# Performance work log

Measured on AMD Instinct MI355X. Metric: run time of the kernel, lower is better.

The kernel has to match this reference:

```python
import math
import jax, jax.numpy as jnp
import numpy as np

LEVELS = 4          # wavelet_levels
PRUNE = 0.05        # wavelet_packet_prune_ratio
EPS = 1e-6
SQRT2 = math.sqrt(2.0)


def _haar_split(c):
    n = c.shape[-1]
    if n % 2 != 0:
        c = jnp.concatenate([c, jnp.zeros(c.shape[:-1] + (1,), c.dtype)], axis=-1)
    even, odd = c[..., 0::2], c[..., 1::2]
    return (even + odd) / SQRT2, (even - odd) / SQRT2, n


def _haar_merge(low, high, orig):
    even = (low + high) / SQRT2
    odd = (low - high) / SQRT2
    out = jnp.stack([even, odd], axis=-1).reshape(*low.shape[:-1], low.shape[-1] * 2)
    return out[..., :orig]


def _coherence(c, gpu):
    unit = c / jnp.maximum(jnp.abs(c), EPS)
    return jnp.clip(jnp.abs(jnp.mean(unit * jnp.conj(gpu), axis=-1, keepdims=True)), 0.0, 1.0)


def _cost(c, gpu):
    # gauge-aware packet cost: Shannon entropy of energy distribution + (1 - coherence)
    if c.shape[-1] <= 1:
        return jnp.float32(0.0)
    e = jnp.square(jnp.abs(c))
    p = jnp.maximum(e / jnp.maximum(e.sum(-1, keepdims=True), EPS), EPS)
    ent = -(p * jnp.log(p)).sum(-1)
    coh = _coherence(c, gpu)[..., 0]
    return jax.lax.stop_gradient(jnp.mean(ent + (1.0 - coh)))


def _band_center(path):
    if not path:
        return 0.0
    idx = 0
    for b in path:
        idx = (idx << 1) | b
    return (idx + 0.5) / (2 ** len(path))


def _leaf_gain(c, path, depth, gpu, Wp, bp, Wo, bo, lfg, sigma, hfg, cutoff):
    mag = jnp.maximum(jnp.abs(c), EPS)
    phase = jnp.arctan2(c.imag, c.real) / math.pi
    nle = jnp.broadcast_to(
        jnp.log(jnp.maximum(jnp.mean(jnp.square(jnp.abs(c)), -1, keepdims=True), EPS)), mag.shape)
    dn = jnp.full(mag.shape, depth / max(1, LEVELS), mag.dtype)
    bcv = _band_center(path)
    bc = jnp.full(mag.shape, bcv, mag.dtype)
    coh = jnp.broadcast_to(_coherence(c, gpu), mag.shape)
    pos = jnp.broadcast_to(jnp.linspace(0.0, 1.0, c.shape[-1], dtype=mag.dtype), mag.shape)
    feats = jnp.stack([jnp.log(mag), phase, nle, dn, bc, coh, pos], axis=-1)  # [..., n, 7]
    gd = jax.nn.silu(feats @ Wp.T + bp) @ Wo.T + bo                            # [..., n, 2]
    dm = 0.25 * jnp.tanh(gd[..., 0])
    dp = 0.5 * math.pi * jnp.tanh(gd[..., 1])
    lbb = 1.0 + lfg * jnp.exp(-(bcv * bcv) / jnp.square(sigma))
    hbd = hfg + (1.0 - hfg) * jax.nn.sigmoid((cutoff - bcv) / sigma)
    gm = lbb * hbd * (1.0 + lfg * coh) * (hfg + (1.0 - hfg) * coh) * jnp.exp(dm)
    return jax.lax.complex(gm * jnp.cos(dp), gm * jnp.sin(dp))  # torch.polar


def _filter_leaf(c, path, depth, total_e, gpu, params):
    Wp, bp, Wo, bo, lfg, sigma, hfg, cutoff = params
    node_e = jax.lax.stop_gradient(jnp.square(jnp.abs(c)).sum())
    filtered = c * _leaf_gain(c, path, depth, gpu, Wp, bp, Wo, bo, lfg, sigma, hfg, cutoff)
    coh_v = jax.lax.stop_gradient(jnp.mean(_coherence(c, gpu)))
    # spectral subtraction
    fm = jnp.abs(filtered)
    nf = jnp.median(fm, axis=-1, keepdims=True)
    damping = hfg + (1.0 - hfg) * jax.nn.sigmoid((cutoff - _band_center(path)) / sigma)
    den = jax.nn.relu(fm - (1.0 - damping) * nf)
    filtered = den * (filtered / jnp.maximum(fm, EPS))
    # prune low-energy / low-coherence leaves
    prune = jnp.logical_or(node_e / total_e < PRUNE, coh_v < PRUNE)
    return jnp.where(prune, filtered * jnp.square(hfg), filtered)


def _apply_node(c, depth, path, total_e, gpu, params):
    cost = _cost(c, gpu)
    leaf = _filter_leaf(c, path, depth, total_e, gpu, params)
    if depth >= LEVELS or c.shape[-1] <= 1:
        return leaf, cost
    low, high, orig = _haar_split(c)
    lr, lc = _apply_node(low, depth + 1, path + (0,), total_e, gpu, params)
    hr, hc = _apply_node(high, depth + 1, path + (1,), total_e, gpu, params)
    merged = _haar_merge(lr, hr, orig)
    child_cost = lc + hc
    # best-basis selection (wavelet_packet_best_basis=True)
    out = jnp.where(child_cost < cost, merged, leaf)
    return out, jnp.minimum(child_cost, cost)


def setup_inputs() -> dict:
    key = jax.random.key(0)
    ks = jax.random.split(key, 3)
    B, R, N = 8, 64, 8192
    x = jax.random.normal(ks[0], (B, R, N), jnp.float32)
    Wp = jax.random.normal(ks[1], (12, 7), jnp.float32) * math.sqrt(2.0 / 19.0)  # xavier-ish
    bp = jnp.zeros((12,), jnp.float32)
    Wo = jax.random.normal(ks[2], (2, 12), jnp.float32) * 0.1
    bo = jnp.zeros((2,), jnp.float32)
    return {"x": x, "Wp": Wp, "bp": bp, "Wo": Wo, "bo": bo,
            "lfg": jnp.float32(0.5), "sigma": jnp.float32(0.3),
            "hfg": jnp.float32(0.7), "cutoff": jnp.float32(0.25)}


def reference(x, Wp, bp, Wo, bo, lfg, sigma, hfg, cutoff):
    n = x.shape[-1]
    spec = jnp.fft.fft(x)  # complex64 [B, R, N]
    # _fft_filter spectral gating
    r2 = jnp.square(jnp.fft.fftfreq(n).astype(x.dtype))
    lfb = 1.0 + lfg * jnp.exp(-r2 / jnp.square(sigma))
    radius = jnp.sqrt(r2 + 1e-12)
    gate = jax.nn.sigmoid((cutoff - radius) / jnp.maximum(sigma, 0.05))
    spec = spec * (lfb * (hfg + (1.0 - hfg) * gate))
    # global phase unit
    unit = spec / jnp.maximum(jnp.abs(spec), EPS)
    g = jnp.mean(unit, axis=-1, keepdims=True)
    gpu = g / jnp.maximum(jnp.abs(g), EPS)
    total_e = jax.lax.stop_gradient(jnp.square(jnp.abs(spec)).sum())
    params = (Wp, bp, Wo, bo, lfg, sigma, hfg, cutoff)
    out, _ = _apply_node(spec, 0, (), total_e, gpu, params)
    return jnp.fft.ifft(out).real
```

## Files before the change

kernel.cpp:

```cpp
#include <hip/hip_runtime.h>
#include <hip/hip_fp16.h>
#include <math.h>

#define NN      8192
#define LOGN    13
#define ROWS    512
#define NT      512
#define NNODES  31
#define EPSF    1e-6f
#define PRUNEF  0.05f
#define SQRT1_2F 0.70710678118654752f
#define PIF      3.14159265358979323f
#define INV_PIF  0.31830988618379067f
#define HALF_PIF 1.57079632679489662f

typedef unsigned int uint;

__device__ __forceinline__ float fast_rcp(float x){ return __builtin_amdgcn_rcpf(x); }
__device__ __forceinline__ float fast_rsq(float x){ return __builtin_amdgcn_rsqf(x); }

__device__ __forceinline__ float tanh_fast(float x){
    float e = __expf(2.f * x);
    return 1.f - 2.f * fast_rcp(e + 1.f);
}
__device__ __forceinline__ float silu_pade(float h){
    float y = fminf(3.f, fmaxf(-3.f, 0.5f * h));
    float y2 = y * y;
    float num = y * fmaf(y2, 10.f, 105.f);
    float den = fmaf(y2, 45.f, fmaf(y2 * y2, 1.f, 105.f));
    return 0.5f * h * (1.f + num * fast_rcp(den));
}
__device__ __forceinline__ float exp_small(float z){
    return fmaf(z, fmaf(z, fmaf(z, fmaf(z, 0.041666667f, 0.16666667f), 0.5f), 1.f), 1.f);
}

__device__ __forceinline__ float fast_atan2f(float y, float x) {
    float ay = fabsf(y), ax = fabsf(x);
    float mx = fmaxf(ax, ay), mn = fminf(ax, ay);
    float a = (mx > 0.f) ? (mn * fast_rcp(mx)) : 0.f;
    bool big = a > 0.4142135679f;
    float t = big ? ((a - 1.f) * fast_rcp(a + 1.f)) : a;
    float z2 = t * t;
    float p = fmaf(8.05374449538e-2f, z2, -1.38776856032e-1f);
    p = fmaf(p, z2, 1.99777106478e-1f);
    p = fmaf(p, z2, -3.33329491539e-1f);
    float r = fmaf(p * z2, t, t);
    if (big) r += 0.78539816339744831f;
    if (ay > ax) r = 1.57079632679489662f - r;
    if (x < 0.f) r = 3.14159265358979323f - r;
    return copysignf(r, y);
}

__device__ __forceinline__ float2 cmul(float2 a, float2 b){
    return make_float2(a.x*b.x - a.y*b.y, a.x*b.y + a.y*b.x);
}
__device__ __forceinline__ float2 cadd(float2 a, float2 b){ return make_float2(a.x+b.x, a.y+b.y); }
__device__ __forceinline__ float2 csub(float2 a, float2 b){ return make_float2(a.x-b.x, a.y-b.y); }

__device__ __forceinline__ uint pack_h2(float2 v){
    __half2 h = __floats2half2_rn(v.x, v.y);
    return __builtin_bit_cast(uint, h);
}
__device__ __forceinline__ float2 unpack_h2(uint u){
    __half2 h = __builtin_bit_cast(__half2, u);
    return make_float2(__low2float(h), __high2float(h));
}

__device__ __forceinline__ void wave_red8(float* a) {
    #pragma unroll
    for (int m = 32; m >= 1; m >>= 1) {
        #pragma unroll
        for (int q = 0; q < 8; ++q) a[q] += __shfl_xor(a[q], m);
    }
}

__global__ __launch_bounds__(NT, 4) void k_pre(
    const float* __restrict__ x, uint* __restrict__ Lv16,
    float* __restrict__ Se, float* __restrict__ Coh, float* __restrict__ Ent,
    const float* lfg_p, const float* sig_p, const float* hfg_p, const float* cut_p)
{
    __shared__ float2 sh[NN];
    __shared__ float4 wred[8];
    __shared__ float nacc[16][4];
    int row = blockIdx.x, tid = threadIdx.x;
    float lfg = *lfg_p, sigma = *sig_p, hfg = *hfg_p, cutoff = *cut_p;

    const float* xr = x + ((size_t)row << LOGN);
    #pragma unroll
    for (int t = 0; t < 16; ++t) {
        int i = tid + (t << 9);
        sh[i] = make_float2(xr[i], 0.f);
    }
    __syncthreads();

    for (int sp = 0; sp < 6; ++sp) {
        int lg = 11 - 2 * sp;
        int Hh = 1 << lg;
        float angf = -PIF / (float)(2 * Hh);
        #pragma unroll 4
        for (int c = 0; c < 4; ++c) {
            int q = tid + (c << 9);
            int j = q & (Hh - 1);
            int p = ((q >> lg) << (lg + 2)) | j;
            float2 a = sh[p], b = sh[p + Hh], cc = sh[p + 2 * Hh], d = sh[p + 3 * Hh];
            float ang = angf * (float)j;
            float s = __sinf(ang), co = __cosf(ang);
            float2 t1 = make_float2(co, s);
            float2 t2 = make_float2(co * co - s * s, 2.f * co * s);
            float2 a1 = cadd(a, cc);
            float2 c1 = cmul(csub(a, cc), t1);
            float2 b1 = cadd(b, d);
            float2 u  = cmul(csub(b, d), t1);
            float2 d1 = make_float2(u.y, -u.x);
            sh[p]          = cadd(a1, b1);
            sh[p + Hh]     = cmul(csub(a1, b1), t2);
            sh[p + 2 * Hh] = cadd(c1, d1);
            sh[p + 3 * Hh] = cmul(csub(c1, d1), t2);
        }
        __syncthreads();
    }
    #pragma unroll 8
    for (int c = 0; c < 8; ++c) {
        int p = (tid + (c << 9)) << 1;
        float2 a = sh[p], b = sh[p + 1];
        sh[p] = cadd(a, b);
        sh[p + 1] = csub(a, b);
    }
    __syncthreads();

    float inv_gs = 1.f / fmaxf(sigma, 0.05f);
    float is2 = 1.f / (sigma * sigma);
    float se = 0.f, slg = 0.f, sux = 0.f, suy = 0.f;
    #pragma unroll
    for (int t = 0; t < 16; ++t) {
        int p = tid + (t << 9);
        int k = (int)(__brev((uint)p) >> 19);
        float fk = (k < NN / 2) ? (float)k : (float)(k - NN);
        float f = fk * (1.0f / (float)NN);
        float r2 = f * f;
        float lfb = 1.f + lfg * __expf(-r2 * is2);
        float radius = sqrtf(r2 + 1e-12f);
        float gate = fast_rcp(1.f + __expf(-(cutoff - radius) * inv_gs));
        float mult = lfb * (hfg + (1.f - hfg) * gate);
        float2 c = sh[p];
        c.x *= mult; c.y *= mult;
        sh[p] = c;
        float e = fmaf(c.x, c.x, c.y * c.y);
        se += e;
        slg += e * __logf(fmaxf(e, 1e-30f));
        float inv = fminf(fast_rsq(e), 1e6f);
        sux += c.x * inv; suy += c.y * inv;
    }
    #pragma unroll
    for (int m = 32; m >= 1; m >>= 1) {
        se += __shfl_xor(se, m); slg += __shfl_xor(slg, m);
        sux += __shfl_xor(sux, m); suy += __shfl_xor(suy, m);
    }
    if ((tid & 63) == 0) wred[tid >> 6] = make_float4(se, slg, sux, suy);
    __syncthreads();
    if (tid == 0) {
        float4 r = wred[0];
        #pragma unroll
        for (int w = 1; w < 8; ++w) {
            r.x += wred[w].x; r.y += wred[w].y; r.z += wred[w].z; r.w += wred[w].w;
        }
        float gx = r.z / (float)NN, gy = r.w / (float)NN;
        float ga = sqrtf(gx * gx + gy * gy);
        float denom = fmaxf(r.x, EPSF);
        Se[row]  = r.x;
        Ent[row] = __logf(denom) - r.y / denom;
        Coh[row] = fminf(ga, 1.f);
    }

    for (int dp = 0; dp < 4; ++dp) {
        int shn = 12 - dp;
        int h = 1 << shn;
        int fim1 = (1 << (3 - dp)) - 1;
        if (tid < 64) ((float*)nacc)[tid] = 0.f;
        __syncthreads();
        float acc[8] = {0,0,0,0,0,0,0,0};
        #pragma unroll
        for (int t = 0; t < 8; ++t) {
            int q = tid + (t << 9);
            int p = ((q & ~(h - 1)) << 1) | (q & (h - 1));
            float2 a = sh[p], b = sh[p + h];
            float2 lo = make_float2((a.x + b.x) * SQRT1_2F, (a.y + b.y) * SQRT1_2F);
            float2 hi = make_float2((a.x - b.x) * SQRT1_2F, (a.y - b.y) * SQRT1_2F);
            sh[p] = lo; sh[p + h] = hi;
            float e1 = fmaf(lo.x, lo.x, lo.y * lo.y);
            acc[0] += e1; acc[1] += e1 * __logf(fmaxf(e1, 1e-30f));
            float i1 = fminf(fast_rsq(e1), 1e6f);
            acc[2] += lo.x * i1; acc[3] += lo.y * i1;
            float e2 = fmaf(hi.x, hi.x, hi.y * hi.y);
            acc[4] += e2; acc[5] += e2 * __logf(fmaxf(e2, 1e-30f));
            float i2 = fminf(fast_rsq(e2), 1e6f);
            acc[6] += hi.x * i2; acc[7] += hi.y * i2;
            if (((t + 1) & fim1) == 0) {
                wave_red8(acc);
                if ((tid & 63) == 0) {
                    int ca = (q >> shn) << 1;
                    atomicAdd(&nacc[ca][0], acc[0]);   atomicAdd(&nacc[ca][1], acc[1]);
                    atomicAdd(&nacc[ca][2], acc[2]);   atomicAdd(&nacc[ca][3], acc[3]);
                    atomicAdd(&nacc[ca+1][0], acc[4]); atomicAdd(&nacc[ca+1][1], acc[5]);
                    atomicAdd(&nacc[ca+1][2], acc[6]); atomicAdd(&nacc[ca+1][3], acc[7]);
                }
                #pragma unroll
                for (int qq = 0; qq < 8; ++qq) acc[qq] = 0.f;
            }
        }
        __syncthreads();
        int cn = 2 << dp;
        if (tid < cn) {
            float E = nacc[tid][0], SL = nacc[tid][1], ZX = nacc[tid][2], ZY = nacc[tid][3];
            float denom = fmaxf(E, EPSF);
            float ent = __logf(denom) - SL / denom;
            float invn = 1.f / (float)(1 << shn);
            float zx = ZX * invn, zy = ZY * invn;
            float ch = fminf(sqrtf(zx * zx + zy * zy), 1.f);
            int g = cn - 1 + tid;
            Se[g * ROWS + row] = E; Coh[g * ROWS + row] = ch; Ent[g * ROWS + row] = ent;
        }
        __syncthreads();
    }

    uint* lrow = Lv16 + ((size_t)row << LOGN);
    #pragma unroll
    for (int t = 0; t < 16; ++t) {
        int k = tid + (t << 9);
        lrow[k] = pack_h2(sh[k]);
    }
}

__global__ __launch_bounds__(NT) void k_decide(
    const float* __restrict__ Se, const float* __restrict__ Coh, const float* __restrict__ Ent,
    int* __restrict__ fFg, int* __restrict__ fPg)
{
    __shared__ float dtmp[3 * NNODES];
    __shared__ int fF[NNODES], fP[NNODES];
    int tid = threadIdx.x;
    float* dcost = dtmp; float* dne = dtmp + NNODES; float* dcm = dtmp + 2 * NNODES;
    int wid = tid >> 6, lane = tid & 63;
    for (int gn = wid; gn < NNODES; gn += 8) {
        float a = 0.f, b = 0.f, cc = 0.f;
        #pragma unroll
        for (int rr = 0; rr < ROWS / 64; ++rr) {
            int r = lane + (rr << 6);
            float ch = Coh[gn * ROWS + r];
            a += Ent[gn * ROWS + r] + 1.f - ch;
            b += Se[gn * ROWS + r];
            cc += ch;
        }
        #pragma unroll
        for (int m = 32; m >= 1; m >>= 1) {
            a += __shfl_xor(a, m); b += __shfl_xor(b, m); cc += __shfl_xor(cc, m);
        }
        if (lane == 0) { dcost[gn] = a / (float)ROWS; dne[gn] = b; dcm[gn] = cc / (float)ROWS; }
    }
    __syncthreads();
    if (tid == 0) {
        float mc[NNODES]; int sel[NNODES]; int act[NNODES];
        for (int gn = NNODES - 1; gn >= 0; --gn) {
            if (gn >= 15) { mc[gn] = dcost[gn]; sel[gn] = 0; }
            else {
                float chc = mc[2 * gn + 1] + mc[2 * gn + 2];
                sel[gn] = (chc < dcost[gn]) ? 1 : 0;
                mc[gn] = fminf(chc, dcost[gn]);
            }
        }
        float total_e = dne[0];
        act[0] = 1;
        for (int gn = 1; gn < NNODES; ++gn) {
            int p = (gn - 1) >> 1;
            act[gn] = act[p] && sel[p];
        }
        for (int gn = 0; gn < NNODES; ++gn) {
            int isleaf = (gn >= 15);
            fF[gn] = (act[gn] && (isleaf || !sel[gn])) ? 1 : 0;
            fP[gn] = ((dne[gn] / total_e < PRUNEF) || (dcm[gn] < PRUNEF)) ? 1 : 0;
        }
    }
    __syncthreads();
    if (tid < NNODES) { fFg[tid] = fF[tid]; fPg[tid] = fP[tid]; }
}

__device__ __forceinline__ uint key_at(const float2* sh, int p) {
    float2 v = sh[p];
    return __float_as_uint(fmaf(v.x, v.x, v.y * v.y));
}

__device__ __forceinline__ uint2 hist_locate1024(
    const uint* hist, int tid, uint r, uint* wsum, uint* selres)
{
    uint l0 = hist[2 * tid], l1 = hist[2 * tid + 1];
    uint s = l0 + l1;
    uint sc = s;
    #pragma unroll
    for (int o = 1; o < 64; o <<= 1) {
        uint v = __shfl_up(sc, o);
        if ((tid & 63) >= o) sc += v;
    }
    int wid = tid >> 6;
    if ((tid & 63) == 63) wsum[wid] = sc;
    __syncthreads();
    uint wb = 0;
    #pragma unroll
    for (int w = 0; w < 8; ++w) if (w < wid) wb += wsum[w];
    uint c0 = wb + sc - s;
    if (r >= c0 && r < c0 + l0) { selres[0] = 2u * tid;      selres[1] = c0; }
    c0 += l0;
    if (r >= c0 && r < c0 + l1) { selres[0] = 2u * tid + 1u; selres[1] = c0; }
    __syncthreads();
    uint2 res = make_uint2(selres[0], selres[1]);
    __syncthreads();
    return res;
}

template<int EPT>
__device__ __forceinline__ float median_node(
    const float2* sh, int nd, int tid,
    uint* hist, uint* wsum, uint* selres)
{
    uint r1 = (uint)(nd / 2 - 1), r2 = (uint)(nd / 2);
    for (int k = tid; k < 1024; k += NT) hist[k] = 0u;
    __syncthreads();
    #pragma unroll
    for (int c = 0; c < EPT; ++c)
        atomicAdd(&hist[key_at(sh, tid + (c << 9)) >> 21], 1u);
    __syncthreads();
    uint2 A1 = hist_locate1024(hist, tid, r1, wsum, selres);
    uint2 A2 = hist_locate1024(hist, tid, r2, wsum, selres);
    uint va, vb;
    if (A1.x != A2.x) {
        if (tid == 0) { selres[0] = 0u; selres[1] = 0xFFFFFFFFu; }
        __syncthreads();
        #pragma unroll
        for (int c = 0; c < EPT; ++c) {
            uint k = key_at(sh, tid + (c << 9));
            uint b = k >> 21;
            if (b == A1.x) atomicMax(&selres[0], k);
            if (b == A2.x) atomicMin(&selres[1], k);
        }
        __syncthreads();
        va = selres[0]; vb = selres[1];
        __syncthreads();
    } else {
        uint p1 = A1.x;
        for (int k = tid; k < 1024; k += NT) hist[k] = 0u;
        __syncthreads();
        #pragma unroll
        for (int c = 0; c < EPT; ++c) {
            uint k = key_at(sh, tid + (c << 9));
            if ((k >> 21) == p1) atomicAdd(&hist[(k >> 11) & 1023u], 1u);
        }
        __syncthreads();
        uint2 B1 = hist_locate1024(hist, tid, r1 - A1.y, wsum, selres);
        uint2 B2 = hist_locate1024(hist, tid, r2 - A1.y, wsum, selres);
        if (B1.x != B2.x) {
            uint pA = (p1 << 10) | B1.x, pB = (p1 << 10) | B2.x;
            if (tid == 0) { selres[0] = 0u; selres[1] = 0xFFFFFFFFu; }
            __syncthreads();
            #pragma unroll
            for (int c = 0; c < EPT; ++c) {
                uint k = key_at(sh, tid + (c << 9));
                uint b = k >> 11;
                if (b == pA) atomicMax(&selres[0], k);
                if (b == pB) atomicMin(&selres[1], k);
            }
            __syncthreads();
            va = selres[0]; vb = selres[1];
            __syncthreads();
        } else {
            uint pfx = (p1 << 10) | B1.x;
            for (int k = tid; k < 1024; k += NT) hist[k] = 0u;
            __syncthreads();
            #pragma unroll
            for (int c = 0; c < EPT; ++c) {
                uint k = key_at(sh, tid + (c << 9));
                if ((k >> 11) == pfx) atomicAdd(&hist[(k >> 1) & 1023u], 1u);
            }
            __syncthreads();
            uint2 C1 = hist_locate1024(hist, tid, r1 - A1.y - B1.y, wsum, selres);
            uint2 C2 = hist_locate1024(hist, tid, r2 - A1.y - B1.y, wsum, selres);
            va = ((pfx << 10) | C1.x) << 1;
            vb = ((pfx << 10) | C2.x) << 1;
        }
    }
    return 0.5f * (sqrtf(__uint_as_float(va)) + sqrtf(__uint_as_float(vb)));
}

template<int D>
__device__ __forceinline__ void filter_node_reg(
    float2 (&v)[16], int n, int tid, float2* sh,
    const float* __restrict__ Wp, const float* __restrict__ bp,
    const float* __restrict__ Wo, const float* __restrict__ bo,
    const float* __restrict__ Se, const float* __restrict__ Coh,
    const int* __restrict__ fPg, int row,
    uint* hist, uint* wsum, uint* selres,
    float lfg, float sigma, float hfg, float cutoff)
{
    constexpr int CNT = 16 >> D;
    constexpr int ND  = NN >> D;
    constexpr int EPT = ND >> 9;
    int g = (1 << D) - 1 + n;

    #pragma unroll
    for (int t = 0; t < 16; ++t) {
        int k = t - n * CNT;
        if ((unsigned)k < (unsigned)CNT) sh[tid + (k << 9)] = v[t];
    }
    __syncthreads();

    float bcv = (D == 0) ? 0.f : ((float)n + 0.5f) / (float)(1 << D);
    float coh = Coh[g * ROWS + row];
    float sev = Se[g * ROWS + row];
    float nle = __logf(fmaxf(sev * (1.f / (float)ND), EPSF));
    float dnv = (float)D * 0.25f;
    float lbb = 1.f + lfg * __expf(-(bcv * bcv) / (sigma * sigma));
    float hbd = hfg + (1.f - hfg) * fast_rcp(1.f + __expf(-(cutoff - bcv) / sigma));
    float gbase = lbb * hbd * (1.f + lfg * coh) * (hfg + (1.f - hfg) * coh);
    float invnm1 = 1.f / (float)(ND - 1);
    float hb[12];
    #pragma unroll
    for (int j = 0; j < 12; ++j)
        hb[j] = bp[j] + nle * Wp[j*7+2] + dnv * Wp[j*7+3] + bcv * Wp[j*7+4] + coh * Wp[j*7+5];
    float bo0 = bo[0], bo1 = bo[1];

    #pragma unroll
    for (int c = 0; c < EPT; ++c) {
        int o = tid + (c << 9);
        float2 cv = sh[o];
        float m2 = fmaf(cv.x, cv.x, cv.y * cv.y);
        float f0 = 0.5f * __logf(fmaxf(m2, 1e-12f));
        float f1 = fast_atan2f(cv.y, cv.x) * INV_PIF;
        int itrue = (int)(__brev((uint)o) >> (19 + D));
        float f6 = (float)itrue * invnm1;
        float acc0 = bo0, acc1 = bo1;
        #pragma unroll
        for (int j = 0; j < 12; ++j) {
            float h = fmaf(f0, Wp[j*7], fmaf(f1, Wp[j*7+1], fmaf(f6, Wp[j*7+6], hb[j])));
            float s = silu_pade(h);
            acc0 = fmaf(s, Wo[j], acc0);
            acc1 = fmaf(s, Wo[12 + j], acc1);
        }
        float gm = gbase * exp_small(0.25f * tanh_fast(acc0));
        float dph = HALF_PIF * tanh_fast(acc1);
        float spv, cpv;
        __sincosf(dph, &spv, &cpv);
        float fr = gm * (cv.x * cpv - cv.y * spv);
        float fi = gm * (cv.x * spv + cv.y * cpv);
        sh[o] = make_float2(fr, fi);
    }
    __syncthreads();

    float nf = median_node<EPT>(sh, ND, tid, hist, wsum, selres);
    float thr = (1.f - hbd) * nf;
    float pf = fPg[g] ? (hfg * hfg) : 1.f;

    #pragma unroll
    for (int c = 0; c < EPT; ++c) {
        int o = tid + (c << 9);
        float2 w = sh[o];
        float fm = sqrtf(fmaf(w.x, w.x, w.y * w.y));
        float den = fmaxf(fm - thr, 0.f);
        float s = den * fast_rcp(fmaxf(fm, EPSF)) * pf;
        sh[o] = make_float2(w.x * s, w.y * s);
    }
    __syncthreads();

    #pragma unroll
    for (int t = 0; t < 16; ++t) {
        int k = t - n * CNT;
        if ((unsigned)k < (unsigned)CNT) v[t] = sh[tid + (k << 9)];
    }
    __syncthreads();
}

template<int DT>
__device__ __forceinline__ void merge_reg(float2 (&v)[16]){
    #pragma unroll
    for (int t = 0; t < 16; ++t) {
        if ((t & DT) == 0) {
            float2 lo = v[t], hi = v[t + DT];
            v[t]      = make_float2((lo.x + hi.x) * SQRT1_2F, (lo.y + hi.y) * SQRT1_2F);
            v[t + DT] = make_float2((lo.x - hi.x) * SQRT1_2F, (lo.y - hi.y) * SQRT1_2F);
        }
    }
}

__global__ __launch_bounds__(NT, 4) void k_rest(
    const uint* __restrict__ Lv16,
    const float* __restrict__ Se, const float* __restrict__ Coh,
    const int* __restrict__ fFg, const int* __restrict__ fPg,
    float* __restrict__ out,
    const float* __restrict__ Wp, const float* __restrict__ bp,
    const float* __restrict__ Wo, const float* __restrict__ bo,
    const float* lfg_p, const float* sig_p, const float* hfg_p, const float* cut_p)
{
    __shared__ float2 sh[NN];
    __shared__ __align__(16) uint hist[1024];
    __shared__ uint wsum[8];
    __shared__ uint selres[2];

    int row = blockIdx.x, tid = threadIdx.x;
    float lfg = *lfg_p, sigma = *sig_p, hfg = *hfg_p, cutoff = *cut_p;

    const uint* lr = Lv16 + ((size_t)row << LOGN);
    uint raw[16];
    #pragma unroll
    for (int t = 0; t < 16; ++t) raw[t] = lr[tid + (t << 9)];

    float2 v[16];
    #pragma unroll
    for (int t = 0; t < 16; ++t) v[t] = unpack_h2(raw[t]);

    for (int n = 0; n < 16; ++n)
        if (fFg[15 + n])
            filter_node_reg<4>(v, n, tid, sh, Wp, bp, Wo, bo, Se, Coh, fPg, row, hist, wsum, selres, lfg, sigma, hfg, cutoff);

    merge_reg<1>(v);
    for (int n = 0; n < 8; ++n)
        if (fFg[7 + n])
            filter_node_reg<3>(v, n, tid, sh, Wp, bp, Wo, bo, Se, Coh, fPg, row, hist, wsum, selres, lfg, sigma, hfg, cutoff);
    merge_reg<2>(v);
    for (int n = 0; n < 4; ++n)
        if (fFg[3 + n])
            filter_node_reg<2>(v, n, tid, sh, Wp, bp, Wo, bo, Se, Coh, fPg, row, hist, wsum, selres, lfg, sigma, hfg, cutoff);
    merge_reg<4>(v);
    for (int n = 0; n < 2; ++n)
        if (fFg[1 + n])
            filter_node_reg<1>(v, n, tid, sh, Wp, bp, Wo, bo, Se, Coh, fPg, row, hist, wsum, selres, lfg, sigma, hfg, cutoff);
    merge_reg<8>(v);
    if (fFg[0])
        filter_node_reg<0>(v, 0, tid, sh, Wp, bp, Wo, bo, Se, Coh, fPg, row, hist, wsum, selres, lfg, sigma, hfg, cutoff);

    #pragma unroll
    for (int t = 0; t < 16; ++t) sh[tid + (t << 9)] = v[t];
    __syncthreads();

    for (int sp = 0; sp < 6; ++sp) {
        int h = 1 << (2 * sp);
        float angf = PIF / (float)(2 * h);
        #pragma unroll 4
        for (int c = 0; c < 4; ++c) {
            int q = tid + (c << 9);
            int jj = q & (h - 1);
            int p0 = ((q >> (2 * sp)) << (2 * sp + 2)) | jj;
            float ang = angf * (float)jj;
            float s2 = __sinf(ang), c2 = __cosf(ang);
            float2 t2 = make_float2(c2, s2);
            float2 t1 = make_float2(c2 * c2 - s2 * s2, 2.f * c2 * s2);
            float2 a = sh[p0], b = sh[p0 + h], cc = sh[p0 + 2 * h], d = sh[p0 + 3 * h];
            float2 tb = cmul(t1, b);
            float2 ap = cadd(a, tb), bp2 = csub(a, tb);
            float2 td = cmul(t1, d);
            float2 cp = cadd(cc, td), dp2 = csub(cc, td);
            float2 tc = cmul(t2, cp);
            float2 u  = cmul(t2, dp2);
            float2 iB = make_float2(-u.y, u.x);
            sh[p0]         = cadd(ap, tc);
            sh[p0 + h]     = cadd(bp2, iB);
            sh[p0 + 2 * h] = csub(ap, tc);
            sh[p0 + 3 * h] = csub(bp2, iB);
        }
        __syncthreads();
    }
    {
        float angf = PIF / 4096.f;
        #pragma unroll 8
        for (int c = 0; c < 8; ++c) {
            int p = tid + (c << 9);
            float ang = angf * (float)p;
            float s = __sinf(ang), co = __cosf(ang);
            float2 a = sh[p], b = sh[p + 4096];
            float2 tb = cmul(make_float2(co, s), b);
            sh[p] = cadd(a, tb);
            sh[p + 4096] = csub(a, tb);
        }
        __syncthreads();
    }
    float* orow = out + ((size_t)row << LOGN);
    #pragma unroll
    for (int t = 0; t < 16; ++t) {
        int i = tid + (t << 9);
        orow[i] = sh[i].x * (1.0f / (float)NN);
    }
}

extern "C" void kernel_launch(void* const* d_in, const int* in_sizes, int n_in,
                              void* d_out, int out_size, void* d_ws, size_t ws_size,
                              hipStream_t stream) {
    const float* x   = (const float*)d_in[0];
    const float* Wp  = (const float*)d_in[1];
    const float* bp  = (const float*)d_in[2];
    const float* Wo  = (const float*)d_in[3];
    const float* bo  = (const float*)d_in[4];
    const float* lfg = (const float*)d_in[5];
    const float* sig = (const float*)d_in[6];
    const float* hfg = (const float*)d_in[7];
    const float* cut = (const float*)d_in[8];
    float* out = (float*)d_out;

    size_t LVB = (size_t)ROWS * NN * sizeof(uint);
    char* ws = (char*)d_ws;
    uint*   Lv16 = (uint*)ws;
    float*  Se   = (float*)(ws + LVB);
    float*  Coh  = Se  + (size_t)NNODES * ROWS;
    float*  Ent  = Coh + (size_t)NNODES * ROWS;
    int*    fFg  = (int*)(Ent + (size_t)NNODES * ROWS);
    int*    fPg  = fFg + NNODES;
    size_t need = (size_t)((char*)(fPg + NNODES) - ws);
    if (ws_size < need) return;

    dim3 b(NT);
    k_pre   <<<dim3(ROWS), b, 0, stream>>>(x, Lv16, Se, Coh, Ent, lfg, sig, hfg, cut);
    k_decide<<<dim3(1),    b, 0, stream>>>(Se, Coh, Ent, fFg, fPg);
    k_rest  <<<dim3(ROWS), b, 0, stream>>>(Lv16, Se, Coh, fFg, fPg, out, Wp, bp, Wo, bo, lfg, sig, hfg, cut);
}
```

Baseline: 139.8 us.

## Keep wavelet split stats in registers and filter root node without shared memory

The k_pre packet-split statistics now run on per-thread register arrays, with one barrier at the end instead of several shared-memory passes per level. The root-node filter in k_rest works on registers directly, using a register-based median histogram instead of staging through shared memory. tanh and sincos are replaced with Pade and polynomial approximations. This removes shared-memory traffic and barriers, at the cost of more register pressure and small accuracy changes from the approximations.

```diff
diff --git a/kernel.cpp b/kernel.cpp
--- a/kernel.cpp
+++ b/kernel.cpp
@@ -19,9 +19,12 @@
 __device__ __forceinline__ float fast_rcp(float x){ return __builtin_amdgcn_rcpf(x); }
 __device__ __forceinline__ float fast_rsq(float x){ return __builtin_amdgcn_rsqf(x); }
 
-__device__ __forceinline__ float tanh_fast(float x){
-    float e = __expf(2.f * x);
-    return 1.f - 2.f * fast_rcp(e + 1.f);
+__device__ __forceinline__ float tanh_pade(float y){
+    y = fminf(3.f, fmaxf(-3.f, y));
+    float y2 = y * y;
+    float num = y * fmaf(y2, 10.f, 105.f);
+    float den = fmaf(y2, 45.f, fmaf(y2 * y2, 1.f, 105.f));
+    return num * fast_rcp(den);
 }
 __device__ __forceinline__ float silu_pade(float h){
     float y = fminf(3.f, fmaxf(-3.f, 0.5f * h));
@@ -32,6 +35,14 @@
 }
 __device__ __forceinline__ float exp_small(float z){
     return fmaf(z, fmaf(z, fmaf(z, fmaf(z, 0.041666667f, 0.16666667f), 0.5f), 1.f), 1.f);
+}
+__device__ __forceinline__ float sin_halfpi(float t){
+    float t2 = t * t;
+    return t * fmaf(t2, fmaf(t2, fmaf(t2, -4.6817541e-3f, 7.96926262e-2f), -6.45964097e-1f), 1.57079632f);
+}
+__device__ __forceinline__ float cos_halfpi(float t){
+    float t2 = t * t;
+    return fmaf(t2, fmaf(t2, fmaf(t2, fmaf(t2, 9.1937e-4f, -2.08634807e-2f), 2.53669508e-1f), -1.23370055f), 1.f);
 }
 
 __device__ __forceinline__ float fast_atan2f(float y, float x) {
@@ -74,6 +85,52 @@
     }
 }
 
+template<int DP>
+__device__ __forceinline__ void level_split_stats(
+    float2 (&v)[16], float* nacc, int tid)
+{
+    constexpr int ST = 8 >> DP;
+    #pragma unroll
+    for (int t = 0; t < 16; ++t) {
+        if ((t & ST) == 0) {
+            float2 a = v[t], b = v[t + ST];
+            v[t]      = make_float2((a.x + b.x) * SQRT1_2F, (a.y + b.y) * SQRT1_2F);
+            v[t + ST] = make_float2((a.x - b.x) * SQRT1_2F, (a.y - b.y) * SQRT1_2F);
+        }
+    }
+    constexpr int CNT = 16 >> (DP + 1);
+    constexpr int NPAIR = 1 << DP;
+    constexpr int G0 = (2 << DP) - 1;
+    #pragma unroll
+    for (int pr = 0; pr < NPAIR; ++pr) {
+        float acc[8] = {0,0,0,0,0,0,0,0};
+        #pragma unroll
+        for (int s = 0; s < CNT; ++s) {
+            float2 w = v[(2 * pr) * CNT + s];
+            float e = fmaf(w.x, w.x, w.y * w.y);
+            acc[0] += e; acc[1] += e * __logf(fmaxf(e, 1e-30f));
+            float iv = fminf(fast_rsq(e), 1e6f);
+            acc[2] += w.x * iv; acc[3] += w.y * iv;
+        }
+        #pragma unroll
+        for (int s = 0; s < CNT; ++s) {
+            float2 w = v[(2 * pr + 1) * CNT + s];
+            float e = fmaf(w.x, w.x, w.y * w.y);
+            acc[4] += e; acc[5] += e * __logf(fmaxf(e, 1e-30f));
+            float iv = fminf(fast_rsq(e), 1e6f);
+            acc[6] += w.x * iv; acc[7] += w.y * iv;
+        }
+        wave_red8(acc);
+        if ((tid & 63) == 0) {
+            int ga = G0 + 2 * pr, gb = ga + 1;
+            atomicAdd(&nacc[(ga - 1) * 4 + 0], acc[0]); atomicAdd(&nacc[(ga - 1) * 4 + 1], acc[1]);
+            atomicAdd(&nacc[(ga - 1) * 4 + 2], acc[2]); atomicAdd(&nacc[(ga - 1) * 4 + 3], acc[3]);
+            atomicAdd(&nacc[(gb - 1) * 4 + 0], acc[4]); atomicAdd(&nacc[(gb - 1) * 4 + 1], acc[5]);
+            atomicAdd(&nacc[(gb - 1) * 4 + 2], acc[6]); atomicAdd(&nacc[(gb - 1) * 4 + 3], acc[7]);
+        }
+    }
+}
+
 __global__ __launch_bounds__(NT, 4) void k_pre(
     const float* __restrict__ x, uint* __restrict__ Lv16,
     float* __restrict__ Se, float* __restrict__ Coh, float* __restrict__ Ent,
@@ -81,7 +138,7 @@
 {
     __shared__ float2 sh[NN];
     __shared__ float4 wred[8];
-    __shared__ float nacc[16][4];
+    __shared__ float nacc[30 * 4];
     int row = blockIdx.x, tid = threadIdx.x;
     float lfg = *lfg_p, sigma = *sig_p, hfg = *hfg_p, cutoff = *cut_p;
 
@@ -128,9 +185,11 @@
     }
     __syncthreads();
 
+    if (tid < 120) nacc[tid] = 0.f;
     float inv_gs = 1.f / fmaxf(sigma, 0.05f);
     float is2 = 1.f / (sigma * sigma);
     float se = 0.f, slg = 0.f, sux = 0.f, suy = 0.f;
+    float2 v[16];
     #pragma unroll
     for (int t = 0; t < 16; ++t) {
         int p = tid + (t << 9);
@@ -144,7 +203,7 @@
         float mult = lfb * (hfg + (1.f - hfg) * gate);
         float2 c = sh[p];
         c.x *= mult; c.y *= mult;
-        sh[p] = c;
+        v[t] = c;
         float e = fmaf(c.x, c.x, c.y * c.y);
         se += e;
         slg += e * __logf(fmaxf(e, 1e-30f));
@@ -172,63 +231,28 @@
         Coh[row] = fminf(ga, 1.f);
     }
 
-    for (int dp = 0; dp < 4; ++dp) {
-        int shn = 12 - dp;
-        int h = 1 << shn;
-        int fim1 = (1 << (3 - dp)) - 1;
-        if (tid < 64) ((float*)nacc)[tid] = 0.f;
-        __syncthreads();
-        float acc[8] = {0,0,0,0,0,0,0,0};
-        #pragma unroll
-        for (int t = 0; t < 8; ++t) {
-            int q = tid + (t << 9);
-            int p = ((q & ~(h - 1)) << 1) | (q & (h - 1));
-            float2 a = sh[p], b = sh[p + h];
-            float2 lo = make_float2((a.x + b.x) * SQRT1_2F, (a.y + b.y) * SQRT1_2F);
-            float2 hi = make_float2((a.x - b.x) * SQRT1_2F, (a.y - b.y) * SQRT1_2F);
-            sh[p] = lo; sh[p + h] = hi;
-            float e1 = fmaf(lo.x, lo.x, lo.y * lo.y);
-            acc[0] += e1; acc[1] += e1 * __logf(fmaxf(e1, 1e-30f));
-            float i1 = fminf(fast_rsq(e1), 1e6f);
-            acc[2] += lo.x * i1; acc[3] += lo.y * i1;
-            float e2 = fmaf(hi.x, hi.x, hi.y * hi.y);
-            acc[4] += e2; acc[5] += e2 * __logf(fmaxf(e2, 1e-30f));
-            float i2 = fminf(fast_rsq(e2), 1e6f);
-            acc[6] += hi.x * i2; acc[7] += hi.y * i2;
-            if (((t + 1) & fim1) == 0) {
-                wave_red8(acc);
-                if ((tid & 63) == 0) {
-                    int ca = (q >> shn) << 1;
-                    atomicAdd(&nacc[ca][0], acc[0]);   atomicAdd(&nacc[ca][1], acc[1]);
-                    atomicAdd(&nacc[ca][2], acc[2]);   atomicAdd(&nacc[ca][3], acc[3]);
-                    atomicAdd(&nacc[ca+1][0], acc[4]); atomicAdd(&nacc[ca+1][1], acc[5]);
-                    atomicAdd(&nacc[ca+1][2], acc[6]); atomicAdd(&nacc[ca+1][3], acc[7]);
-                }
-                #pragma unroll
-                for (int qq = 0; qq < 8; ++qq) acc[qq] = 0.f;
-            }
-        }
-        __syncthreads();
-        int cn = 2 << dp;
-        if (tid < cn) {
-            float E = nacc[tid][0], SL = nacc[tid][1], ZX = nacc[tid][2], ZY = nacc[tid][3];
-            float denom = fmaxf(E, EPSF);
-            float ent = __logf(denom) - SL / denom;
-            float invn = 1.f / (float)(1 << shn);
-            float zx = ZX * invn, zy = ZY * invn;
-            float ch = fminf(sqrtf(zx * zx + zy * zy), 1.f);
-            int g = cn - 1 + tid;
-            Se[g * ROWS + row] = E; Coh[g * ROWS + row] = ch; Ent[g * ROWS + row] = ent;
-        }
-        __syncthreads();
+    level_split_stats<0>(v, nacc, tid);
+    level_split_stats<1>(v, nacc, tid);
+    level_split_stats<2>(v, nacc, tid);
+    level_split_stats<3>(v, nacc, tid);
+    __syncthreads();
+    if (tid < 30) {
+        int g = tid + 1;
+        float E = nacc[tid * 4 + 0], SL = nacc[tid * 4 + 1];
+        float ZX = nacc[tid * 4 + 2], ZY = nacc[tid * 4 + 3];
+        float denom = fmaxf(E, EPSF);
+        float ent = __logf(denom) - SL / denom;
+        int d = 31 - __clz(g + 1);
+        float invn = 1.f / (float)(NN >> d);
+        float zx = ZX * invn, zy = ZY * invn;
+        float ch = fminf(sqrtf(zx * zx + zy * zy), 1.f);
+        Se[g * ROWS + row] = E; Coh[g * ROWS + row] = ch; Ent[g * ROWS + row] = ent;
     }
 
     uint* lrow = Lv16 + ((size_t)row << LOGN);
     #pragma unroll
-    for (int t = 0; t < 16; ++t) {
-        int k = tid + (t << 9);
-        lrow[k] = pack_h2(sh[k]);
-    }
+    for (int t = 0; t < 16; ++t)
+        lrow[tid + (t << 9)] = pack_h2(v[t]);
 }
 
 __global__ __launch_bounds__(NT) void k_decide(
@@ -283,10 +307,10 @@
     if (tid < NNODES) { fFg[tid] = fF[tid]; fPg[tid] = fP[tid]; }
 }
 
-__device__ __forceinline__ uint key_at(const float2* sh, int p) {
-    float2 v = sh[p];
+__device__ __forceinline__ uint key_of(float2 v) {
     return __float_as_uint(fmaf(v.x, v.x, v.y * v.y));
 }
+__device__ __forceinline__ uint key_at(const float2* sh, int p) { return key_of(sh[p]); }
 
 __device__ __forceinline__ uint2 hist_locate1024(
     const uint* hist, int tid, uint r, uint* wsum, uint* selres)
@@ -388,8 +412,130 @@
     return 0.5f * (sqrtf(__uint_as_float(va)) + sqrtf(__uint_as_float(vb)));
 }
 
+__device__ __forceinline__ float median_root_reg(
+    const float2 (&v)[16], int tid, uint* hist, uint* wsum, uint* selres)
+{
+    const uint r1 = NN / 2 - 1, r2 = NN / 2;
+    for (int k = tid; k < 1024; k += NT) hist[k] = 0u;
+    __syncthreads();
+    #pragma unroll
+    for (int t = 0; t < 16; ++t)
+        atomicAdd(&hist[key_of(v[t]) >> 21], 1u);
+    __syncthreads();
+    uint2 A1 = hist_locate1024(hist, tid, r1, wsum, selres);
+    uint2 A2 = hist_locate1024(hist, tid, r2, wsum, selres);
+    uint va, vb;
+    if (A1.x != A2.x) {
+        if (tid == 0) { selres[0] = 0u; selres[1] = 0xFFFFFFFFu; }
+        __syncthreads();
+        #pragma unroll
+        for (int t = 0; t < 16; ++t) {
+            uint k = key_of(v[t]);
+            uint b = k >> 21;
+            if (b == A1.x) atomicMax(&selres[0], k);
+            if (b == A2.x) atomicMin(&selres[1], k);
+        }
+        __syncthreads();
+        va = selres[0]; vb = selres[1];
+        __syncthreads();
+    } else {
+        uint p1 = A1.x;
+        for (int k = tid; k < 1024; k += NT) hist[k] = 0u;
+        __syncthreads();
+        #pragma unroll
+        for (int t = 0; t < 16; ++t) {
+            uint k = key_of(v[t]);
+            if ((k >> 21) == p1) atomicAdd(&hist[(k >> 11) & 1023u], 1u);
+        }
+        __syncthreads();
+        uint2 B1 = hist_locate1024(hist, tid, r1 - A1.y, wsum, selres);
+        uint2 B2 = hist_locate1024(hist, tid, r2 - A1.y, wsum, selres);
+        if (B1.x != B2.x) {
+            uint pA = (p1 << 10) | B1.x, pB = (p1 << 10) | B2.x;
+            if (tid == 0) { selres[0] = 0u; selres[1] = 0xFFFFFFFFu; }
+            __syncthreads();
+            #pragma unroll
+            for (int t = 0; t < 16; ++t) {
+                uint k = key_of(v[t]);
+                uint b = k >> 11;
+                if (b == pA) atomicMax(&selres[0], k);
+                if (b == pB) atomicMin(&selres[1], k);
+            }
+            __syncthreads();
+            va = selres[0]; vb = selres[1];
+            __syncthreads();
+        } else {
+            uint pfx = (p1 << 10) | B1.x;
+            for (int k = tid; k < 1024; k += NT) hist[k] = 0u;
+            __syncthreads();
+            #pragma unroll
+            for (int t = 0; t < 16; ++t) {
+                uint k = key_of(v[t]);
+                if ((k >> 11) == pfx) atomicAdd(&hist[(k >> 1) & 1023u], 1u);
+            }
+            __syncthreads();
+            uint2 C1 = hist_locate1024(hist, tid, r1 - A1.y - B1.y, wsum, selres);
+            uint2 C2 = hist_locate1024(hist, tid, r2 - A1.y - B1.y, wsum, selres);
+            va = ((pfx << 10) | C1.x) << 1;
+            vb = ((pfx << 10) | C2.x) << 1;
+        }
+    }
+    return 0.5f * (sqrtf(__uint_as_float(va)) + sqrtf(__uint_as_float(vb)));
+}
+
+struct NodeConst {
+    float hbd, gbase, hb[12], bo0, bo1;
+};
+__device__ __forceinline__ NodeConst node_consts(
+    int D, int nodes, int n, int g, int ND, int row,
+    const float* __restrict__ Wp, const float* __restrict__ bp,
+    const float* __restrict__ Wo, const float* __restrict__ bo,
+    const float* __restrict__ Se, const float* __restrict__ Coh,
+    float lfg, float sigma, float hfg, float cutoff, float& coh_o)
+{
+    NodeConst nc;
+    float bcv = (D == 0) ? 0.f : ((float)n + 0.5f) / (float)nodes;
+    float coh = Coh[g * ROWS + row];
+    float sev = Se[g * ROWS + row];
+    float nle = __logf(fmaxf(sev * (1.f / (float)ND), EPSF));
+    float dnv = (float)D * 0.25f;
+    float lbb = 1.f + lfg * __expf(-(bcv * bcv) / (sigma * sigma));
+    nc.hbd = hfg + (1.f - hfg) * fast_rcp(1.f + __expf(-(cutoff - bcv) / sigma));
+    nc.gbase = lbb * nc.hbd * (1.f + lfg * coh) * (hfg + (1.f - hfg) * coh);
+    #pragma unroll
+    for (int j = 0; j < 12; ++j)
+        nc.hb[j] = bp[j] + nle * Wp[j*7+2] + dnv * Wp[j*7+3] + bcv * Wp[j*7+4] + coh * Wp[j*7+5];
+    nc.bo0 = bo[0]; nc.bo1 = bo[1];
+    coh_o = coh;
+    return nc;
+}
+
+__device__ __forceinline__ float2 mlp_apply(
+    float2 cv, int o, int D, float invnm1, const NodeConst& nc,
+    const float* __restrict__ Wp, const float* __restrict__ Wo)
+{
+    float m2 = fmaf(cv.x, cv.x, cv.y * cv.y);
+    float f0 = 0.5f * __logf(fmaxf(m2, 1e-12f));
+    float f1 = fast_atan2f(cv.y, cv.x) * INV_PIF;
+    int itrue = (int)(__brev((uint)o) >> (19 + D));
+    float f6 = (float)itrue * invnm1;
+    float acc0 = nc.bo0, acc1 = nc.bo1;
+    #pragma unroll
+    for (int j = 0; j < 12; ++j) {
+        float h = fmaf(f0, Wp[j*7], fmaf(f1, Wp[j*7+1], fmaf(f6, Wp[j*7+6], nc.hb[j])));
+        float s = silu_pade(h);
+        acc0 = fmaf(s, Wo[j], acc0);
+        acc1 = fmaf(s, Wo[12 + j], acc1);
+    }
+    float gm = nc.gbase * exp_small(0.25f * tanh_pade(acc0));
+    float tp = tanh_pade(acc1);
+    float spv = sin_halfpi(tp), cpv = cos_halfpi(tp);
+    return make_float2(gm * (cv.x * cpv - cv.y * spv),
+                       gm * (cv.x * spv + cv.y * cpv));
+}
+
 template<int D>
-__device__ __forceinline__ void filter_node_reg(
+__device__ __forceinline__ void filter_node_sh(
     float2 (&v)[16], int n, int tid, float2* sh,
     const float* __restrict__ Wp, const float* __restrict__ bp,
     const float* __restrict__ Wo, const float* __restrict__ bo,
@@ -410,50 +556,20 @@
     }
     __syncthreads();
 
-    float bcv = (D == 0) ? 0.f : ((float)n + 0.5f) / (float)(1 << D);
-    float coh = Coh[g * ROWS + row];
-    float sev = Se[g * ROWS + row];
-    float nle = __logf(fmaxf(sev * (1.f / (float)ND), EPSF));
-    float dnv = (float)D * 0.25f;
-    float lbb = 1.f + lfg * __expf(-(bcv * bcv) / (sigma * sigma));
-    float hbd = hfg + (1.f - hfg) * fast_rcp(1.f + __expf(-(cutoff - bcv) / sigma));
-    float gbase = lbb * hbd * (1.f + lfg * coh) * (hfg + (1.f - hfg) * coh);
+    float coh;
+    NodeConst nc = node_consts(D, 1 << D, n, g, ND, row, Wp, bp, Wo, bo, Se, Coh,
+                               lfg, sigma, hfg, cutoff, coh);
     float invnm1 = 1.f / (float)(ND - 1);
-    float hb[12];
-    #pragma unroll
-    for (int j = 0; j < 12; ++j)
-        hb[j] = bp[j] + nle * Wp[j*7+2] + dnv * Wp[j*7+3] + bcv * Wp[j*7+4] + coh * Wp[j*7+5];
-    float bo0 = bo[0], bo1 = bo[1];
 
     #pragma unroll
     for (int c = 0; c < EPT; ++c) {
         int o = tid + (c << 9);
-        float2 cv = sh[o];
-        float m2 = fmaf(cv.x, cv.x, cv.y * cv.y);
-        float f0 = 0.5f * __logf(fmaxf(m2, 1e-12f));
-        float f1 = fast_atan2f(cv.y, cv.x) * INV_PIF;
-        int itrue = (int)(__brev((uint)o) >> (19 + D));
-        float f6 = (float)itrue * invnm1;
-        float acc0 = bo0, acc1 = bo1;
-        #pragma unroll
-        for (int j = 0; j < 12; ++j) {
-            float h = fmaf(f0, Wp[j*7], fmaf(f1, Wp[j*7+1], fmaf(f6, Wp[j*7+6], hb[j])));
-            float s = silu_pade(h);
-            acc0 = fmaf(s, Wo[j], acc0);
-            acc1 = fmaf(s, Wo[12 + j], acc1);
-        }
-        float gm = gbase * exp_small(0.25f * tanh_fast(acc0));
-        float dph = HALF_PIF * tanh_fast(acc1);
-        float spv, cpv;
-        __sincosf(dph, &spv, &cpv);
-        float fr = gm * (cv.x * cpv - cv.y * spv);
-        float fi = gm * (cv.x * spv + cv.y * cpv);
-        sh[o] = make_float2(fr, fi);
+        sh[o] = mlp_apply(sh[o], o, D, invnm1, nc, Wp, Wo);
     }
     __syncthreads();
 
     float nf = median_node<EPT>(sh, ND, tid, hist, wsum, selres);
-    float thr = (1.f - hbd) * nf;
+    float thr = (1.f - nc.hbd) * nf;
     float pf = fPg[g] ? (hfg * hfg) : 1.f;
 
     #pragma unroll
@@ -473,6 +589,40 @@
         if ((unsigned)k < (unsigned)CNT) v[t] = sh[tid + (k << 9)];
     }
     __syncthreads();
+}
+
+__device__ __forceinline__ void filter_root_reg(
+    float2 (&v)[16], int tid,
+    const float* __restrict__ Wp, const float* __restrict__ bp,
+    const float* __restrict__ Wo, const float* __restrict__ bo,
+    const float* __restrict__ Se, const float* __restrict__ Coh,
+    const int* __restrict__ fPg, int row,
+    uint* hist, uint* wsum, uint* selres,
+    float lfg, float sigma, float hfg, float cutoff)
+{
+    float coh;
+    NodeConst nc = node_consts(0, 1, 0, 0, NN, row, Wp, bp, Wo, bo, Se, Coh,
+                               lfg, sigma, hfg, cutoff, coh);
+    float invnm1 = 1.f / (float)(NN - 1);
+
+    #pragma unroll
+    for (int t = 0; t < 16; ++t) {
+        int o = tid + (t << 9);
+        v[t] = mlp_apply(v[t], o, 0, invnm1, nc, Wp, Wo);
+    }
+
+    float nf = median_root_reg(v, tid, hist, wsum, selres);
+    float thr = (1.f - nc.hbd) * nf;
+    float pf = fPg[0] ? (hfg * hfg) : 1.f;
+
+    #pragma unroll
+    for (int t = 0; t < 16; ++t) {
+        float2 w = v[t];
+        float fm = sqrtf(fmaf(w.x, w.x, w.y * w.y));
+        float den = fmaxf(fm - thr, 0.f);
+        float s = den * fast_rcp(fmaxf(fm, EPSF)) * pf;
+        v[t] = make_float2(w.x * s, w.y * s);
+    }
 }
 
 template<int DT>
@@ -515,23 +665,23 @@
 
     for (int n = 0; n < 16; ++n)
         if (fFg[15 + n])
-            filter_node_reg<4>(v, n, tid, sh, Wp, bp, Wo, bo, Se, Coh, fPg, row, hist, wsum, selres, lfg, sigma, hfg, cutoff);
+            filter_node_sh<4>(v, n, tid, sh, Wp, bp, Wo, bo, Se, Coh, fPg, row, hist, wsum, selres, lfg, sigma, hfg, cutoff);
 
     merge_reg<1>(v);
     for (int n = 0; n < 8; ++n)
         if (fFg[7 + n])
-            filter_node_reg<3>(v, n, tid, sh, Wp, bp, Wo, bo, Se, Coh, fPg, row, hist, wsum, selres, lfg, sigma, hfg, cutoff);
+            filter_node_sh<3>(v, n, tid, sh, Wp, bp, Wo, bo, Se, Coh, fPg, row, hist, wsum, selres, lfg, sigma, hfg, cutoff);
     merge_reg<2>(v);
     for (int n = 0; n < 4; ++n)
         if (fFg[3 + n])
-            filter_node_reg<2>(v, n, tid, sh, Wp, bp, Wo, bo, Se, Coh, fPg, row, hist, wsum, selres, lfg, sigma, hfg, cutoff);
+            filter_node_sh<2>(v, n, tid, sh, Wp, bp, Wo, bo, Se, Coh, fPg, row, hist, wsum, selres, lfg, sigma, hfg, cutoff);
     merge_reg<4>(v);
     for (int n = 0; n < 2; ++n)
         if (fFg[1 + n])
-            filter_node_reg<1>(v, n, tid, sh, Wp, bp, Wo, bo, Se, Coh, fPg, row, hist, wsum, selres, lfg, sigma, hfg, cutoff);
+            filter_node_sh<1>(v, n, tid, sh, Wp, bp, Wo, bo, Se, Coh, fPg, row, hist, wsum, selres, lfg, sigma, hfg, cutoff);
     merge_reg<8>(v);
     if (fFg[0])
-        filter_node_reg<0>(v, 0, tid, sh, Wp, bp, Wo, bo, Se, Coh, fPg, row, hist, wsum, selres, lfg, sigma, hfg, cutoff);
+        filter_root_reg(v, tid, Wp, bp, Wo, bo, Se, Coh, fPg, row, hist, wsum, selres, lfg, sigma, hfg, cutoff);
 
     #pragma unroll
     for (int t = 0; t < 16; ++t) sh[tid + (t << 9)] = v[t];
```

Result: faster. 131.8 us (-5.7%).
